# Kernel optimization log

Measured on AMD Instinct MI355X. Metric: run time of the kernel, lower is better.

## Reference

```python
import jax, jax.numpy as jnp
import numpy as np


def conv1x1(x, w, b):
    # x: (B,C,H,W), w: (O,C), b: (O,) -- 1x1 conv == channel matmul
    return jnp.einsum('bchw,oc->bohw', x, w) + b[None, :, None, None]


def setup_inputs() -> dict:
    key = jax.random.key(0)
    B, C, H, W = 4, 256, 64, 64
    Ch = C // 2
    ks = jax.random.split(key, 12)
    s = 0.05
    return {
        'x':    jax.random.normal(ks[0], (B, C, H, W), jnp.float32),
        'wf1':  jax.random.normal(ks[1], (Ch, C), jnp.float32) * s,
        'bf1':  jnp.zeros((Ch,), jnp.float32),
        'wf2':  jax.random.normal(ks[2], (Ch, Ch), jnp.float32) * s,
        'bf2':  jnp.zeros((Ch,), jnp.float32),
        'wg1':  jax.random.normal(ks[3], (Ch, C), jnp.float32) * s,
        'bg1':  jnp.zeros((Ch,), jnp.float32),
        'wg2':  jax.random.normal(ks[4], (Ch, Ch), jnp.float32) * s,
        'bg2':  jnp.zeros((Ch,), jnp.float32),
        'wh':   jax.random.normal(ks[5], (C, C), jnp.float32) * s,
        'bh':   jnp.zeros((C,), jnp.float32),
        'gamma': jnp.full((1,), 0.5, jnp.float32),
    }


def reference(x, wf1, bf1, wf2, bf2, wg1, bg1, wg2, bg2, wh, bh, gamma):
    B, C, H, W = x.shape
    N = H * W
    # f_ and g_: conv1x1 -> relu -> conv1x1, projecting C -> C/2
    f = conv1x1(jax.nn.relu(conv1x1(x, wf1, bf1)), wf2, bf2).reshape(B, -1, N)  # (B,C/2,N)
    g = conv1x1(jax.nn.relu(conv1x1(x, wg1, bg1)), wg2, bg2).reshape(B, -1, N)  # (B,C/2,N)
    h = conv1x1(x, wh, bh).reshape(B, C, N)                                     # (B,C,N)
    # attn_dist = bmm(f^T, g): (B, N, N)
    attn = jnp.einsum('bcn,bcm->bnm', f, g)
    # softmax over dim=1 (the query axis) -- non-standard axis, as in source
    attn_soft = jax.nn.softmax(attn, axis=1)
    out = jnp.einsum('bcn,bnm->bcm', h, attn_soft).reshape(B, C, H, W)
    out = gamma[0] * out + x  # skip connection
    return out, attn_soft.reshape(B, H, W, N)
```

## Files before the change

### kernel.cpp

```cpp
#include <hip/hip_runtime.h>

typedef unsigned short u16;
typedef unsigned int   u32;
typedef float  floatx4 __attribute__((ext_vector_type(4)));
typedef __bf16 bfx8    __attribute__((ext_vector_type(8)));
typedef u16    u16x8   __attribute__((ext_vector_type(8)));

#define DEV __device__ __forceinline__

#define NB 4
#define NC 256
#define NCH 128
#define NSP 4096
#define OUT_OFF 4194304

DEV u16 f2bf(float f) {
  u32 u = __builtin_bit_cast(u32, f);
  u = (u + 0x7fffu + ((u >> 16) & 1u)) >> 16;
  return (u16)u;
}

DEV void lds_load16(const u16* g, u16* l) {
  __builtin_amdgcn_global_load_lds(
      (const __attribute__((address_space(1))) u32*)g,
      (__attribute__((address_space(3))) u32*)l, 16, 0, 0);
}

DEV floatx4 mfma16(bfx8 a, bfx8 b, floatx4 c) {
  return __builtin_amdgcn_mfma_f32_16x16x32_bf16(a, b, c, 0, 0, 0);
}

DEV float rsum16(float v) {
  #pragma unroll
  for (int m = 1; m < 16; m <<= 1) v += __shfl_xor(v, m, 64);
  return v;
}

__global__ __launch_bounds__(256) void cvt_all(
    const float* __restrict__ a0, const float* __restrict__ a1,
    const float* __restrict__ a2, const float* __restrict__ a3,
    const float* __restrict__ a4,
    u16* __restrict__ o0, u16* __restrict__ o1, u16* __restrict__ o2,
    u16* __restrict__ o3, u16* __restrict__ o4) {
  int i = blockIdx.x * 256 + threadIdx.x;
  if (i < 32768) { o0[i] = f2bf(a0[i]); return; }
  i -= 32768;
  if (i < 16384) { o1[i] = f2bf(a1[i]); return; }
  i -= 16384;
  if (i < 32768) { o2[i] = f2bf(a2[i]); return; }
  i -= 32768;
  if (i < 16384) { o3[i] = f2bf(a3[i]); return; }
  i -= 16384;
  o4[i] = f2bf(a4[i]);
}

__global__ __launch_bounds__(256) void zero_f(float* __restrict__ p, int n) {
  int i = blockIdx.x * 256 + threadIdx.x;
  if (i < n) p[i] = 0.f;
}

__global__ __launch_bounds__(256) void transpose_x(const float* __restrict__ x,
                                                   u16* __restrict__ xT) {
  __shared__ float T[64 * 65];
  const int b = blockIdx.z, c0 = blockIdx.y * 64, n0 = blockIdx.x * 64;
  const int tid = threadIdx.x;
  const int j = tid & 63, r0 = tid >> 6;
  const size_t xbase = ((size_t)b * NC + c0) * NSP + n0;
  #pragma unroll
  for (int s = 0; s < 16; s++) {
    int cl = s * 4 + r0;
    T[cl * 65 + j] = x[xbase + (size_t)cl * NSP + j];
  }
  __syncthreads();
  const size_t tbase = ((size_t)b * NSP + n0) * NC + c0;
  #pragma unroll
  for (int s = 0; s < 16; s++) {
    int nr = s * 4 + r0;
    xT[tbase + (size_t)nr * NC + j] = f2bf(T[j * 65 + nr]);
  }
}

template<int BM, int BN, int BK, int BIAS, bool RELU, bool OUTBF16, bool FINAL>
__global__ __launch_bounds__(256) void gemm_bt_k(
    const u16* __restrict__ A, long long sA, int lda,
    const u16* __restrict__ Bt, long long sB, int ldb,
    void* __restrict__ C, long long sC, int ldc,
    int K, const float* __restrict__ bias,
    const float* __restrict__ gamma, const float* __restrict__ xres) {
  constexpr int TM = BM / 32, TN = BN / 32, KS = BK / 32;
  __shared__ u16 As[BM * BK];
  __shared__ u16 Bs[BN * BK];
  const int b = blockIdx.z;
  const u16* Ab = A + (size_t)sA * b;
  const u16* Bb = Bt + (size_t)sB * b;
  const int m0 = blockIdx.x * BM, n0 = blockIdx.y * BN;
  const int tid = threadIdx.x, lane = tid & 63, wave = tid >> 6;
  const int q = lane >> 4, cc = lane & 15;
  const int wm = (wave >> 1) * (BM / 2), wn = (wave & 1) * (BN / 2);

  floatx4 acc[TM][TN];
  #pragma unroll
  for (int mi = 0; mi < TM; mi++)
    #pragma unroll
    for (int ni = 0; ni < TN; ni++)
      acc[mi][ni] = floatx4{0.f, 0.f, 0.f, 0.f};

  for (int k0 = 0; k0 < K; k0 += BK) {
    #pragma unroll
    for (int i = 0; i < BM * BK / 2048; i++) {
      int slot = i * 256 + tid;
      int fr = slot / (64 * KS);
      int ks = (slot / 64) % KS;
      int qq = (slot >> 4) & 3, cq = slot & 15;
      lds_load16(Ab + (size_t)(m0 + fr * 16 + cq) * lda + k0 + ks * 32 + qq * 8,
                 As + slot * 8);
    }
    #pragma unroll
    for (int i = 0; i < BN * BK / 2048; i++) {
      int slot = i * 256 + tid;
      int fr = slot / (64 * KS);
      int ks = (slot / 64) % KS;
      int qq = (slot >> 4) & 3, cq = slot & 15;
      lds_load16(Bb + (size_t)(n0 + fr * 16 + cq) * ldb + k0 + ks * 32 + qq * 8,
                 Bs + slot * 8);
    }
    __syncthreads();
    #pragma unroll
    for (int ks = 0; ks < KS; ks++) {
      bfx8 af[TM], bfr[TN];
      #pragma unroll
      for (int mi = 0; mi < TM; mi++)
        af[mi] = *(const bfx8*)(As + ((((wm >> 4) + mi) * KS + ks) * 64 + lane) * 8);
      #pragma unroll
      for (int ni = 0; ni < TN; ni++)
        bfr[ni] = *(const bfx8*)(Bs + ((((wn >> 4) + ni) * KS + ks) * 64 + lane) * 8);
      #pragma unroll
      for (int mi = 0; mi < TM; mi++)
        #pragma unroll
        for (int ni = 0; ni < TN; ni++)
          acc[mi][ni] = mfma16(af[mi], bfr[ni], acc[mi][ni]);
    }
    __syncthreads();
  }

  float g0 = 0.f;
  if constexpr (FINAL) g0 = gamma[0];
  #pragma unroll
  for (int mi = 0; mi < TM; mi++) {
    #pragma unroll
    for (int ni = 0; ni < TN; ni++) {
      #pragma unroll
      for (int r = 0; r < 4; r++) {
        int row = m0 + wm + mi * 16 + q * 4 + r;
        int col = n0 + wn + ni * 16 + cc;
        float v = acc[mi][ni][r];
        if constexpr (BIAS == 1) v += bias[col];
        if constexpr (BIAS == 2) v += bias[row];
        if constexpr (RELU) v = fmaxf(v, 0.f);
        if constexpr (FINAL)
          v = g0 * v + xres[(size_t)sC * b + (size_t)row * ldc + col];
        size_t idx = (size_t)sC * b + (size_t)row * ldc + col;
        if constexpr (OUTBF16) ((u16*)C)[idx] = f2bf(v);
        else ((float*)C)[idx] = v;
      }
    }
  }
}

__global__ __launch_bounds__(256) void attn_rowsum_k(
    const u16* __restrict__ gT, const u16* __restrict__ fT,
    float* __restrict__ rsum) {
  __shared__ u16 Bs[64 * 128];
  const int b = blockIdx.z, m0 = blockIdx.y * 64, n0 = blockIdx.x * 512;
  const int tid = threadIdx.x, lane = tid & 63, wave = tid >> 6;
  const int q = lane >> 4, cc = lane & 15;
  const size_t bN = (size_t)b * NSP;

  bfx8 af[4];
  {
    const u16* gA = gT + (bN + m0 + wave * 16 + cc) * NCH;
    #pragma unroll
    for (int ks = 0; ks < 4; ks++) af[ks] = *(const bfx8*)(gA + ks * 32 + q * 8);
  }
  float ps[4] = {0.f, 0.f, 0.f, 0.f};

  for (int sc = 0; sc < 8; sc++) {
    const int nc = n0 + sc * 64;
    #pragma unroll
    for (int i = 0; i < 4; i++) {
      int slot = i * 256 + tid;
      int ni = slot >> 8, ks = (slot >> 6) & 3;
      int qq = (slot >> 4) & 3, cq = slot & 15;
      lds_load16(fT + (bN + nc + ni * 16 + cq) * NCH + ks * 32 + qq * 8,
                 Bs + slot * 8);
    }
    __syncthreads();
    #pragma unroll
    for (int ni = 0; ni < 4; ni++) {
      floatx4 s = floatx4{0.f, 0.f, 0.f, 0.f};
      #pragma unroll
      for (int ks = 0; ks < 4; ks++) {
        bfx8 bfr = *(const bfx8*)(Bs + ((ni * 4 + ks) * 64 + lane) * 8);
        s = mfma16(af[ks], bfr, s);
      }
      #pragma unroll
      for (int r = 0; r < 4; r++) ps[r] += __expf(fminf(s[r], 80.f));
    }
    __syncthreads();
  }
  #pragma unroll
  for (int r = 0; r < 4; r++) ps[r] = rsum16(ps[r]);
  if (cc == 0) {
    #pragma unroll
    for (int r = 0; r < 4; r++)
      atomicAdd(&rsum[bN + m0 + wave * 16 + q * 4 + r], ps[r]);
  }
}

__global__ __launch_bounds__(256) void attn_p_k(
    const u16* __restrict__ gT, const u16* __restrict__ fT,
    const float* __restrict__ rsum,
    float* __restrict__ outP, u16* __restrict__ pT) {
  __shared__ u16 Bs[64 * 128];
  __shared__ float Pt[64 * 68];
  __shared__ u16 Pb[64 * 72];
  const int b = blockIdx.z, m0 = blockIdx.y * 64, n0 = blockIdx.x * 256;
  const int tid = threadIdx.x, lane = tid & 63, wave = tid >> 6;
  const int q = lane >> 4, cc = lane & 15;
  const size_t bN = (size_t)b * NSP;

  bfx8 af[4];
  {
    const u16* gA = gT + (bN + m0 + wave * 16 + cc) * NCH;
    #pragma unroll
    for (int ks = 0; ks < 4; ks++) af[ks] = *(const bfx8*)(gA + ks * 32 + q * 8);
  }
  float rinvv[4];
  #pragma unroll
  for (int r = 0; r < 4; r++)
    rinvv[r] = 1.f / rsum[bN + m0 + wave * 16 + q * 4 + r];

  for (int sc = 0; sc < 4; sc++) {
    const int nc = n0 + sc * 64;
    #pragma unroll
    for (int i = 0; i < 4; i++) {
      int slot = i * 256 + tid;
      int ni = slot >> 8, ks = (slot >> 6) & 3;
      int qq = (slot >> 4) & 3, cq = slot & 15;
      lds_load16(fT + (bN + nc + ni * 16 + cq) * NCH + ks * 32 + qq * 8,
                 Bs + slot * 8);
    }
    __syncthreads();
    #pragma unroll
    for (int ni = 0; ni < 4; ni++) {
      floatx4 s = floatx4{0.f, 0.f, 0.f, 0.f};
      #pragma unroll
      for (int ks = 0; ks < 4; ks++) {
        bfx8 bfr = *(const bfx8*)(Bs + ((ni * 4 + ks) * 64 + lane) * 8);
        s = mfma16(af[ks], bfr, s);
      }
      #pragma unroll
      for (int r = 0; r < 4; r++) {
        float p = __expf(fminf(s[r], 80.f)) * rinvv[r];
        int ml = wave * 16 + q * 4 + r;
        int nl = ni * 16 + cc;
        Pt[nl * 68 + ml] = p;
        Pb[ml * 72 + nl] = f2bf(p);
      }
    }
    __syncthreads();
    #pragma unroll
    for (int i = 0; i < 4; i++) {
      int slot = i * 256 + tid;
      int nl = slot >> 4, f4 = slot & 15;
      floatx4 v = *(const floatx4*)(Pt + nl * 68 + f4 * 4);
      *(floatx4*)(outP + (bN + nc + nl) * NSP + m0 + f4 * 4) = v;
    }
    #pragma unroll
    for (int i = 0; i < 2; i++) {
      int slot = i * 256 + tid;
      int ml = slot >> 3, c8 = slot & 7;
      u16x8 v = *(const u16x8*)(Pb + ml * 72 + c8 * 8);
      *(u16x8*)(pT + (bN + m0 + ml) * NSP + nc + c8 * 8) = v;
    }
    __syncthreads();
  }
}

extern "C" void kernel_launch(void* const* d_in, const int* in_sizes, int n_in,
                              void* d_out, int out_size, void* d_ws, size_t ws_size,
                              hipStream_t stream) {
  const float* x     = (const float*)d_in[0];
  const float* wf1   = (const float*)d_in[1];
  const float* bf1   = (const float*)d_in[2];
  const float* wf2   = (const float*)d_in[3];
  const float* bf2   = (const float*)d_in[4];
  const float* wg1   = (const float*)d_in[5];
  const float* bg1   = (const float*)d_in[6];
  const float* wg2   = (const float*)d_in[7];
  const float* bg2   = (const float*)d_in[8];
  const float* wh    = (const float*)d_in[9];
  const float* bh    = (const float*)d_in[10];
  const float* gamma = (const float*)d_in[11];
  float* out = (float*)d_out;

  char* ws = (char*)d_ws;
  size_t off = 0;
  auto alloc = [&](size_t bytes) -> char* {
    char* p = ws + off;
    off += (bytes + 255) & ~(size_t)255;
    return p;
  };
  u16* wf1b = (u16*)alloc((size_t)NCH * NC * 2);
  u16* wf2b = (u16*)alloc((size_t)NCH * NCH * 2);
  u16* wg1b = (u16*)alloc((size_t)NCH * NC * 2);
  u16* wg2b = (u16*)alloc((size_t)NCH * NCH * 2);
  u16* whb  = (u16*)alloc((size_t)NC * NC * 2);
  u16* xT   = (u16*)alloc((size_t)NB * NSP * NC * 2);
  u16* f1T  = (u16*)alloc((size_t)NB * NSP * NCH * 2);
  u16* g1T  = (u16*)alloc((size_t)NB * NSP * NCH * 2);
  u16* fTb  = (u16*)alloc((size_t)NB * NSP * NCH * 2);
  u16* gTb  = (u16*)alloc((size_t)NB * NSP * NCH * 2);
  u16* hb   = (u16*)alloc((size_t)NB * NC * NSP * 2);
  float* rs = (float*)alloc((size_t)NB * NSP * 4);
  u16* pTb  = (u16*)alloc((size_t)NB * NSP * NSP * 2);

  cvt_all<<<dim3(640), 256, 0, stream>>>(wf1, wf2, wg1, wg2, wh,
                                         wf1b, wf2b, wg1b, wg2b, whb);
  transpose_x<<<dim3(NSP / 64, NC / 64, NB), 256, 0, stream>>>(x, xT);
  zero_f<<<dim3(NB * NSP / 256), 256, 0, stream>>>(rs, NB * NSP);

  const long long sX = (long long)NSP * NC;
  const long long sH = (long long)NC * NSP;
  const long long sP = (long long)NSP * NSP;

  gemm_bt_k<64, 128, 32, 1, true, true, false><<<dim3(256, 1, 1), 256, 0, stream>>>(
      xT, 0, NC, wf1b, 0, NC, f1T, 0, NCH, NC, bf1, nullptr, nullptr);
  gemm_bt_k<64, 128, 32, 1, true, true, false><<<dim3(256, 1, 1), 256, 0, stream>>>(
      xT, 0, NC, wg1b, 0, NC, g1T, 0, NCH, NC, bg1, nullptr, nullptr);
  gemm_bt_k<64, 128, 32, 1, false, true, false><<<dim3(256, 1, 1), 256, 0, stream>>>(
      f1T, 0, NCH, wf2b, 0, NCH, fTb, 0, NCH, NCH, bf2, nullptr, nullptr);
  gemm_bt_k<64, 128, 32, 1, false, true, false><<<dim3(256, 1, 1), 256, 0, stream>>>(
      g1T, 0, NCH, wg2b, 0, NCH, gTb, 0, NCH, NCH, bg2, nullptr, nullptr);
  gemm_bt_k<64, 128, 32, 2, false, true, false><<<dim3(4, 32, NB), 256, 0, stream>>>(
      whb, 0, NC, xT, sX, NC, hb, sH, NSP, NC, bh, nullptr, nullptr);

  attn_rowsum_k<<<dim3(8, 64, NB), 256, 0, stream>>>(gTb, fTb, rs);
  attn_p_k<<<dim3(16, 64, NB), 256, 0, stream>>>(gTb, fTb, rs, out + OUT_OFF, pTb);

  gemm_bt_k<128, 64, 64, 0, false, false, true><<<dim3(2, 64, NB), 256, 0, stream>>>(
      hb, sH, NSP, pTb, sP, NSP, out, sH, NSP, NSP, nullptr, gamma, x);

  (void)in_sizes; (void)n_in; (void)out_size; (void)ws_size;
}
```

Before: 543.7 us.

## Store unnormalized exp once, defer softmax normalization to final GEMM and separate pass

Merges the rowsum and P-generation attention kernels into one pass that computes the scores once, writes unnormalized bf16 exponentials and accumulates the row sums. The normalization is moved into the final GEMM epilogue, which scales per column by gamma/rowsum, and into a new transpose kernel that rebuilds the fp32 attention output from the bf16 buffer. The f/g projection GEMMs are batched into single launches with concatenated weights and biases, and the final GEMM gets a block-index swizzle. The goal is to remove the duplicate score GEMM and exp pass, at the cost of re-reading the bf16 P buffer. The fp32 attention output now comes from bf16-rounded values, which lowers its precision.

```diff
diff --git a/kernel.cpp b/kernel.cpp
--- a/kernel.cpp
+++ b/kernel.cpp
@@ -37,26 +37,37 @@
 }
 
 __global__ __launch_bounds__(256) void cvt_all(
-    const float* __restrict__ a0, const float* __restrict__ a1,
-    const float* __restrict__ a2, const float* __restrict__ a3,
-    const float* __restrict__ a4,
-    u16* __restrict__ o0, u16* __restrict__ o1, u16* __restrict__ o2,
-    u16* __restrict__ o3, u16* __restrict__ o4) {
+    const float* __restrict__ wf1, const float* __restrict__ wg1,
+    const float* __restrict__ wf2, const float* __restrict__ wg2,
+    const float* __restrict__ wh,
+    u16* __restrict__ wfg1b, u16* __restrict__ wfg2b, u16* __restrict__ whb) {
   int i = blockIdx.x * 256 + threadIdx.x;
-  if (i < 32768) { o0[i] = f2bf(a0[i]); return; }
+  if (i < 32768) { wfg1b[i] = f2bf(wf1[i]); return; }
   i -= 32768;
-  if (i < 16384) { o1[i] = f2bf(a1[i]); return; }
+  if (i < 32768) { wfg1b[32768 + i] = f2bf(wg1[i]); return; }
+  i -= 32768;
+  if (i < 16384) { wfg2b[i] = f2bf(wf2[i]); return; }
   i -= 16384;
-  if (i < 32768) { o2[i] = f2bf(a2[i]); return; }
-  i -= 32768;
-  if (i < 16384) { o3[i] = f2bf(a3[i]); return; }
+  if (i < 16384) { wfg2b[16384 + i] = f2bf(wg2[i]); return; }
   i -= 16384;
-  o4[i] = f2bf(a4[i]);
-}
-
-__global__ __launch_bounds__(256) void zero_f(float* __restrict__ p, int n) {
+  whb[i] = f2bf(wh[i]);
+}
+
+__global__ __launch_bounds__(256) void prep_k(
+    float* __restrict__ rs,
+    const float* __restrict__ bf1, const float* __restrict__ bg1,
+    const float* __restrict__ bf2, const float* __restrict__ bg2,
+    float* __restrict__ bfg1, float* __restrict__ bfg2) {
   int i = blockIdx.x * 256 + threadIdx.x;
-  if (i < n) p[i] = 0.f;
+  if (i < NB * NSP) { rs[i] = 0.f; return; }
+  i -= NB * NSP;
+  if (i < 128) { bfg1[i] = bf1[i]; return; }
+  i -= 128;
+  if (i < 128) { bfg1[128 + i] = bg1[i]; return; }
+  i -= 128;
+  if (i < 128) { bfg2[i] = bf2[i]; return; }
+  i -= 128;
+  if (i < 128) { bfg2[128 + i] = bg2[i]; return; }
 }
 
 __global__ __launch_bounds__(256) void transpose_x(const float* __restrict__ x,
@@ -80,20 +91,33 @@
   }
 }
 
-template<int BM, int BN, int BK, int BIAS, bool RELU, bool OUTBF16, bool FINAL>
+template<int BM, int BN, int BK, int BIAS, bool RELU, bool OUTBF16, bool FINAL,
+         bool SWZ>
 __global__ __launch_bounds__(256) void gemm_bt_k(
     const u16* __restrict__ A, long long sA, int lda,
     const u16* __restrict__ Bt, long long sB, int ldb,
     void* __restrict__ C, long long sC, int ldc,
-    int K, const float* __restrict__ bias,
-    const float* __restrict__ gamma, const float* __restrict__ xres) {
+    int K, const float* __restrict__ bias, int sbias,
+    const float* __restrict__ gamma, const float* __restrict__ xres,
+    const float* __restrict__ rsv) {
   constexpr int TM = BM / 32, TN = BN / 32, KS = BK / 32;
   __shared__ u16 As[BM * BK];
   __shared__ u16 Bs[BN * BK];
-  const int b = blockIdx.z;
+  int bx = blockIdx.x, by = blockIdx.y, bz = blockIdx.z;
+  if constexpr (SWZ) {
+    const int gx = gridDim.x, gy = gridDim.y;
+    const int nwg = gx * gy * gridDim.z;
+    const int bid = (bz * gy + by) * gx + bx;
+    const int lx = (bid & 7) * (nwg >> 3) + (bid >> 3);
+    bx = lx % gx;
+    const int t = lx / gx;
+    by = t % gy;
+    bz = t / gy;
+  }
+  const int b = bz;
   const u16* Ab = A + (size_t)sA * b;
   const u16* Bb = Bt + (size_t)sB * b;
-  const int m0 = blockIdx.x * BM, n0 = blockIdx.y * BN;
+  const int m0 = bx * BM, n0 = by * BN;
   const int tid = threadIdx.x, lane = tid & 63, wave = tid >> 6;
   const int q = lane >> 4, cc = lane & 15;
   const int wm = (wave >> 1) * (BM / 2), wn = (wave & 1) * (BN / 2);
@@ -149,17 +173,18 @@
   for (int mi = 0; mi < TM; mi++) {
     #pragma unroll
     for (int ni = 0; ni < TN; ni++) {
+      const int col = n0 + wn + ni * 16 + cc;
+      float scl = 0.f;
+      if constexpr (FINAL) scl = g0 / rsv[(size_t)b * NSP + col];
       #pragma unroll
       for (int r = 0; r < 4; r++) {
         int row = m0 + wm + mi * 16 + q * 4 + r;
-        int col = n0 + wn + ni * 16 + cc;
         float v = acc[mi][ni][r];
-        if constexpr (BIAS == 1) v += bias[col];
-        if constexpr (BIAS == 2) v += bias[row];
+        if constexpr (BIAS == 1) v += bias[b * sbias + col];
+        if constexpr (BIAS == 2) v += bias[b * sbias + row];
         if constexpr (RELU) v = fmaxf(v, 0.f);
-        if constexpr (FINAL)
-          v = g0 * v + xres[(size_t)sC * b + (size_t)row * ldc + col];
         size_t idx = (size_t)sC * b + (size_t)row * ldc + col;
+        if constexpr (FINAL) v = v * scl + xres[idx];
         if constexpr (OUTBF16) ((u16*)C)[idx] = f2bf(v);
         else ((float*)C)[idx] = v;
       }
@@ -167,10 +192,11 @@
   }
 }
 
-__global__ __launch_bounds__(256) void attn_rowsum_k(
+__global__ __launch_bounds__(256) void attn_se_k(
     const u16* __restrict__ gT, const u16* __restrict__ fT,
-    float* __restrict__ rsum) {
+    float* __restrict__ rsum, u16* __restrict__ pT) {
   __shared__ u16 Bs[64 * 128];
+  __shared__ u16 Pb[64 * 72];
   const int b = blockIdx.z, m0 = blockIdx.y * 64, n0 = blockIdx.x * 512;
   const int tid = threadIdx.x, lane = tid & 63, wave = tid >> 6;
   const int q = lane >> 4, cc = lane & 15;
@@ -204,78 +230,13 @@
         s = mfma16(af[ks], bfr, s);
       }
       #pragma unroll
-      for (int r = 0; r < 4; r++) ps[r] += __expf(fminf(s[r], 80.f));
+      for (int r = 0; r < 4; r++) {
+        float e = __expf(fminf(s[r], 80.f));
+        ps[r] += e;
+        Pb[(wave * 16 + q * 4 + r) * 72 + ni * 16 + cc] = f2bf(e);
+      }
     }
     __syncthreads();
-  }
-  #pragma unroll
-  for (int r = 0; r < 4; r++) ps[r] = rsum16(ps[r]);
-  if (cc == 0) {
-    #pragma unroll
-    for (int r = 0; r < 4; r++)
-      atomicAdd(&rsum[bN + m0 + wave * 16 + q * 4 + r], ps[r]);
-  }
-}
-
-__global__ __launch_bounds__(256) void attn_p_k(
-    const u16* __restrict__ gT, const u16* __restrict__ fT,
-    const float* __restrict__ rsum,
-    float* __restrict__ outP, u16* __restrict__ pT) {
-  __shared__ u16 Bs[64 * 128];
-  __shared__ float Pt[64 * 68];
-  __shared__ u16 Pb[64 * 72];
-  const int b = blockIdx.z, m0 = blockIdx.y * 64, n0 = blockIdx.x * 256;
-  const int tid = threadIdx.x, lane = tid & 63, wave = tid >> 6;
-  const int q = lane >> 4, cc = lane & 15;
-  const size_t bN = (size_t)b * NSP;
-
-  bfx8 af[4];
-  {
-    const u16* gA = gT + (bN + m0 + wave * 16 + cc) * NCH;
-    #pragma unroll
-    for (int ks = 0; ks < 4; ks++) af[ks] = *(const bfx8*)(gA + ks * 32 + q * 8);
-  }
-  float rinvv[4];
-  #pragma unroll
-  for (int r = 0; r < 4; r++)
-    rinvv[r] = 1.f / rsum[bN + m0 + wave * 16 + q * 4 + r];
-
-  for (int sc = 0; sc < 4; sc++) {
-    const int nc = n0 + sc * 64;
-    #pragma unroll
-    for (int i = 0; i < 4; i++) {
-      int slot = i * 256 + tid;
-      int ni = slot >> 8, ks = (slot >> 6) & 3;
-      int qq = (slot >> 4) & 3, cq = slot & 15;
-      lds_load16(fT + (bN + nc + ni * 16 + cq) * NCH + ks * 32 + qq * 8,
-                 Bs + slot * 8);
-    }
-    __syncthreads();
-    #pragma unroll
-    for (int ni = 0; ni < 4; ni++) {
-      floatx4 s = floatx4{0.f, 0.f, 0.f, 0.f};
-      #pragma unroll
-      for (int ks = 0; ks < 4; ks++) {
-        bfx8 bfr = *(const bfx8*)(Bs + ((ni * 4 + ks) * 64 + lane) * 8);
-        s = mfma16(af[ks], bfr, s);
-      }
-      #pragma unroll
-      for (int r = 0; r < 4; r++) {
-        float p = __expf(fminf(s[r], 80.f)) * rinvv[r];
-        int ml = wave * 16 + q * 4 + r;
-        int nl = ni * 16 + cc;
-        Pt[nl * 68 + ml] = p;
-        Pb[ml * 72 + nl] = f2bf(p);
-      }
-    }
-    __syncthreads();
-    #pragma unroll
-    for (int i = 0; i < 4; i++) {
-      int slot = i * 256 + tid;
-      int nl = slot >> 4, f4 = slot & 15;
-      floatx4 v = *(const floatx4*)(Pt + nl * 68 + f4 * 4);
-      *(floatx4*)(outP + (bN + nc + nl) * NSP + m0 + f4 * 4) = v;
-    }
     #pragma unroll
     for (int i = 0; i < 2; i++) {
       int slot = i * 256 + tid;
@@ -283,7 +244,44 @@
       u16x8 v = *(const u16x8*)(Pb + ml * 72 + c8 * 8);
       *(u16x8*)(pT + (bN + m0 + ml) * NSP + nc + c8 * 8) = v;
     }
-    __syncthreads();
+  }
+  #pragma unroll
+  for (int r = 0; r < 4; r++) ps[r] = rsum16(ps[r]);
+  if (cc == 0) {
+    #pragma unroll
+    for (int r = 0; r < 4; r++)
+      atomicAdd(&rsum[bN + m0 + wave * 16 + q * 4 + r], ps[r]);
+  }
+}
+
+__global__ __launch_bounds__(256) void attn_norm_k(
+    const u16* __restrict__ pT, const float* __restrict__ rs,
+    float* __restrict__ outP) {
+  __shared__ float T[64 * 65];
+  const int b = blockIdx.z, n0 = blockIdx.x * 64, m0 = blockIdx.y * 64;
+  const int tid = threadIdx.x;
+  const size_t bN = (size_t)b * NSP;
+  #pragma unroll
+  for (int i = 0; i < 2; i++) {
+    int slot = i * 256 + tid;
+    int ml = slot >> 3, c8 = slot & 7;
+    u16x8 v = *(const u16x8*)(pT + (bN + m0 + ml) * NSP + n0 + c8 * 8);
+    float rinv = 1.f / rs[bN + m0 + ml];
+    #pragma unroll
+    for (int j = 0; j < 8; j++) {
+      u32 w = (u32)v[j] << 16;
+      T[ml * 65 + c8 * 8 + j] = __builtin_bit_cast(float, w) * rinv;
+    }
+  }
+  __syncthreads();
+  #pragma unroll
+  for (int i = 0; i < 4; i++) {
+    int slot = i * 256 + tid;
+    int nl = slot >> 4, f4 = slot & 15;
+    floatx4 o;
+    #pragma unroll
+    for (int k = 0; k < 4; k++) o[k] = T[(f4 * 4 + k) * 65 + nl];
+    *(floatx4*)(outP + (bN + n0 + nl) * NSP + m0 + f4 * 4) = o;
   }
 }
 
@@ -311,45 +309,51 @@
     off += (bytes + 255) & ~(size_t)255;
     return p;
   };
-  u16* wf1b = (u16*)alloc((size_t)NCH * NC * 2);
-  u16* wf2b = (u16*)alloc((size_t)NCH * NCH * 2);
-  u16* wg1b = (u16*)alloc((size_t)NCH * NC * 2);
-  u16* wg2b = (u16*)alloc((size_t)NCH * NCH * 2);
-  u16* whb  = (u16*)alloc((size_t)NC * NC * 2);
+  u16* wfg1b = (u16*)alloc((size_t)256 * 256 * 2);
+  u16* wfg2b = (u16*)alloc((size_t)2 * 128 * 128 * 2);
+  u16* whb   = (u16*)alloc((size_t)NC * NC * 2);
+  float* bfg1 = (float*)alloc(256 * 4);
+  float* bfg2 = (float*)alloc(256 * 4);
   u16* xT   = (u16*)alloc((size_t)NB * NSP * NC * 2);
-  u16* f1T  = (u16*)alloc((size_t)NB * NSP * NCH * 2);
-  u16* g1T  = (u16*)alloc((size_t)NB * NSP * NCH * 2);
+  u16* fg1T = (u16*)alloc((size_t)NB * NSP * 256 * 2);
   u16* fTb  = (u16*)alloc((size_t)NB * NSP * NCH * 2);
   u16* gTb  = (u16*)alloc((size_t)NB * NSP * NCH * 2);
   u16* hb   = (u16*)alloc((size_t)NB * NC * NSP * 2);
   float* rs = (float*)alloc((size_t)NB * NSP * 4);
   u16* pTb  = (u16*)alloc((size_t)NB * NSP * NSP * 2);
 
-  cvt_all<<<dim3(640), 256, 0, stream>>>(wf1, wf2, wg1, wg2, wh,
-                                         wf1b, wf2b, wg1b, wg2b, whb);
+  cvt_all<<<dim3(640), 256, 0, stream>>>(wf1, wg1, wf2, wg2, wh,
+                                         wfg1b, wfg2b, whb);
+  prep_k<<<dim3(66), 256, 0, stream>>>(rs, bf1, bg1, bf2, bg2, bfg1, bfg2);
   transpose_x<<<dim3(NSP / 64, NC / 64, NB), 256, 0, stream>>>(x, xT);
-  zero_f<<<dim3(NB * NSP / 256), 256, 0, stream>>>(rs, NB * NSP);
 
   const long long sX = (long long)NSP * NC;
   const long long sH = (long long)NC * NSP;
   const long long sP = (long long)NSP * NSP;
-
-  gemm_bt_k<64, 128, 32, 1, true, true, false><<<dim3(256, 1, 1), 256, 0, stream>>>(
-      xT, 0, NC, wf1b, 0, NC, f1T, 0, NCH, NC, bf1, nullptr, nullptr);
-  gemm_bt_k<64, 128, 32, 1, true, true, false><<<dim3(256, 1, 1), 256, 0, stream>>>(
-      xT, 0, NC, wg1b, 0, NC, g1T, 0, NCH, NC, bg1, nullptr, nullptr);
-  gemm_bt_k<64, 128, 32, 1, false, true, false><<<dim3(256, 1, 1), 256, 0, stream>>>(
-      f1T, 0, NCH, wf2b, 0, NCH, fTb, 0, NCH, NCH, bf2, nullptr, nullptr);
-  gemm_bt_k<64, 128, 32, 1, false, true, false><<<dim3(256, 1, 1), 256, 0, stream>>>(
-      g1T, 0, NCH, wg2b, 0, NCH, gTb, 0, NCH, NCH, bg2, nullptr, nullptr);
-  gemm_bt_k<64, 128, 32, 2, false, true, false><<<dim3(4, 32, NB), 256, 0, stream>>>(
-      whb, 0, NC, xT, sX, NC, hb, sH, NSP, NC, bh, nullptr, nullptr);
-
-  attn_rowsum_k<<<dim3(8, 64, NB), 256, 0, stream>>>(gTb, fTb, rs);
-  attn_p_k<<<dim3(16, 64, NB), 256, 0, stream>>>(gTb, fTb, rs, out + OUT_OFF, pTb);
-
-  gemm_bt_k<128, 64, 64, 0, false, false, true><<<dim3(2, 64, NB), 256, 0, stream>>>(
-      hb, sH, NSP, pTb, sP, NSP, out, sH, NSP, NSP, nullptr, gamma, x);
+  const long long sFG = (long long)NB * NSP * NCH;
+
+  gemm_bt_k<64, 128, 64, 1, true, true, false, false>
+      <<<dim3(256, 2, 1), 256, 0, stream>>>(
+      xT, 0, NC, wfg1b, 0, NC, fg1T, 0, 256, NC, bfg1, 0,
+      nullptr, nullptr, nullptr);
+  gemm_bt_k<64, 128, 64, 1, false, true, false, false>
+      <<<dim3(256, 1, 2), 256, 0, stream>>>(
+      fg1T, 128, 256, wfg2b, 128 * 128, NCH, fTb, sFG, NCH, NCH, bfg2, 128,
+      nullptr, nullptr, nullptr);
+  gemm_bt_k<64, 128, 64, 2, false, true, false, false>
+      <<<dim3(4, 32, NB), 256, 0, stream>>>(
+      whb, 0, NC, xT, sX, NC, hb, sH, NSP, NC, bh, 0,
+      nullptr, nullptr, nullptr);
+
+  attn_se_k<<<dim3(8, 64, NB), 256, 0, stream>>>(gTb, fTb, rs, pTb);
+
+  gemm_bt_k<128, 64, 64, 0, false, false, true, true>
+      <<<dim3(2, 64, NB), 256, 0, stream>>>(
+      hb, sH, NSP, pTb, sP, NSP, out, sH, NSP, NSP, nullptr, 0,
+      gamma, x, rs);
+
+  attn_norm_k<<<dim3(NSP / 64, NSP / 64, NB), 256, 0, stream>>>(
+      pTb, rs, out + OUT_OFF);
 
   (void)in_sizes; (void)n_in; (void)out_size; (void)ws_size;
 }
```

New measurement: 495.9 us. 8.8% less time.
